# Performance work log

Measured on AMD Instinct MI355X. Metric: run time of the kernel, lower is better.

Reference implementation:

```python
import jax, jax.numpy as jnp
import numpy as np

N, E, F_IN, H, C, L = 100000, 1000000, 500, 64, 3, 3
EPS_MSG = 1e-7   # GENConv message eps
LN_EPS = 1e-5    # torch LayerNorm default eps


def layernorm(x, g, b):
    mu = jnp.mean(x, axis=-1, keepdims=True)
    var = jnp.var(x, axis=-1, keepdims=True)
    return (x - mu) * jax.lax.rsqrt(var + LN_EPS) * g + b


def gen_conv(x, src, dst, W1, b1, g1, be1, W2, b2, t):
    # message: relu(x_j) + eps   (no edge_attr)
    m = jax.nn.relu(x[src]) + EPS_MSG                      # [E, H]
    # softmax aggregation with learnable temperature t (per-channel over edges of each dst node)
    z = m * t
    zmax = jax.ops.segment_max(z, dst, num_segments=N)     # [N, H]
    a = jnp.exp(z - zmax[dst])                             # [E, H]
    denom = jax.ops.segment_sum(a, dst, num_segments=N)    # [N, H]
    agg = jax.ops.segment_sum(m * (a / denom[dst]), dst, num_segments=N)
    # out = mlp(aggr + x_root); MLP = Lin(H,2H) -> LN -> ReLU -> Lin(2H,H)
    h = agg + x
    h1 = jax.nn.relu(layernorm(h @ W1 + b1, g1, be1))
    return h1 @ W2 + b2


def setup_inputs() -> dict:
    key = jax.random.key(0)
    ks = jax.random.split(key, 16)
    s = lambda *sh: 1.0 / np.sqrt(sh[-2] if len(sh) > 1 else 1.0)
    inp = {
        'x': jax.random.normal(ks[0], (N, F_IN), dtype=jnp.float32),
        'edge_index': jax.random.randint(ks[1], (2, E), 0, N, dtype=jnp.int64),
        'enc_W': jax.random.normal(ks[2], (F_IN, H), dtype=jnp.float32) / np.sqrt(F_IN),
        'enc_b': jnp.zeros((H,), jnp.float32),
        'W1': jax.random.normal(ks[3], (L, H, 2 * H), dtype=jnp.float32) / np.sqrt(H),
        'b1': jnp.zeros((L, 2 * H), jnp.float32),
        'g1': jnp.ones((L, 2 * H), jnp.float32),
        'be1': jnp.zeros((L, 2 * H), jnp.float32),
        'W2': jax.random.normal(ks[4], (L, 2 * H, H), dtype=jnp.float32) / np.sqrt(2 * H),
        'b2': jnp.zeros((L, H), jnp.float32),
        't': jnp.ones((L,), jnp.float32),
        'ng': jnp.ones((L, H), jnp.float32),
        'nb': jnp.zeros((L, H), jnp.float32),
        'lin_W': jax.random.normal(ks[5], (H, C), dtype=jnp.float32) / np.sqrt(H),
        'lin_b': jnp.zeros((C,), jnp.float32),
    }
    return inp


def reference(x, edge_index, enc_W, enc_b, W1, b1, g1, be1, W2, b2, t, ng, nb, lin_W, lin_b):
    src, dst = edge_index[0], edge_index[1]
    h = x @ enc_W + enc_b
    # forward applies layers[0].conv once before the loop
    h = gen_conv(h, src, dst, W1[0], b1[0], g1[0], be1[0], W2[0], b2[0], t[0])
    # DeepGCNLayer block='res': h = x + dropout(relu(norm(conv(x)))), dropout is identity in eval
    for l in range(L):
        c = gen_conv(h, src, dst, W1[l], b1[l], g1[l], be1[l], W2[l], b2[l], t[l])
        c = jax.nn.relu(layernorm(c, ng[l], nb[l]))
        h = h + c
    h = jax.nn.relu(layernorm(h, ng[0], nb[0]))
    return h @ lin_W + lin_b
```

## Files before the change

kernel.cpp:

```cpp
#include <hip/hip_runtime.h>
#include <hip/hip_bf16.h>
#include <math.h>

constexpr int GN_N  = 100000;
constexpr int GN_E  = 1000000;
constexpr int GN_F  = 500;
constexpr int GN_H  = 64;
constexpr int GN_2H = 128;
constexpr int GN_C  = 3;
constexpr float GN_EPS_MSG = 1e-7f;
constexpr float GN_LN_EPS  = 1e-5f;

__global__ void k_prep(int* __restrict__ cursor, const long long* __restrict__ e64,
                       int* __restrict__ flag) {
    int i = blockIdx.x * blockDim.x + threadIdx.x;
    if (i < GN_N) cursor[i] = 0;
    if (blockIdx.x == 0) {
        __shared__ int ok;
        if (threadIdx.x == 0) ok = 1;
        __syncthreads();
        long long v = e64[threadIdx.x];
        if (v < 0 || v >= (long long)GN_N) ok = 0;
        __syncthreads();
        if (threadIdx.x == 0) *flag = ok;
    }
}

__global__ void k_hist(const void* eidx, const int* __restrict__ flag,
                       int* __restrict__ deg) {
    int e = blockIdx.x * blockDim.x + threadIdx.x;
    if (e >= GN_E) return;
    int d;
    if (*flag) d = (int)((const long long*)eidx)[GN_E + e];
    else       d = ((const int*)eidx)[GN_E + e];
    atomicAdd(&deg[d], 1);
}

__global__ void k_scan1(const int* __restrict__ deg, int* __restrict__ rowptr,
                        int* __restrict__ blksums) {
    __shared__ int sh[1024];
    int tid = threadIdx.x;
    int i = blockIdx.x * 1024 + tid;
    int v = (i < GN_N) ? deg[i] : 0;
    sh[tid] = v;
    __syncthreads();
    for (int o = 1; o < 1024; o <<= 1) {
        int add = (tid >= o) ? sh[tid - o] : 0;
        __syncthreads();
        sh[tid] += add;
        __syncthreads();
    }
    if (i < GN_N) rowptr[i + 1] = sh[tid];
    if (tid == 1023) blksums[blockIdx.x] = sh[1023];
}

__global__ void k_scan2(int* __restrict__ blksums, int nblk) {
    __shared__ int sh[128];
    int tid = threadIdx.x;
    int v = (tid < nblk) ? blksums[tid] : 0;
    sh[tid] = v;
    __syncthreads();
    for (int o = 1; o < 128; o <<= 1) {
        int add = (tid >= o) ? sh[tid - o] : 0;
        __syncthreads();
        sh[tid] += add;
        __syncthreads();
    }
    if (tid < nblk) blksums[tid] = sh[tid] - v;
}

__global__ void k_scan3(int* __restrict__ rowptr, int* __restrict__ cursor,
                        const int* __restrict__ blksums) {
    int i = blockIdx.x * 1024 + threadIdx.x;
    if (i < GN_N) {
        int v = rowptr[i + 1] + blksums[blockIdx.x];
        rowptr[i + 1] = v;
        cursor[i + 1] = v;
    }
    if (i == 0) { rowptr[0] = 0; cursor[0] = 0; }
}

__global__ void k_scatter(const void* eidx, const int* __restrict__ flag,
                          int* __restrict__ cursor, int* __restrict__ csr_src) {
    int e = blockIdx.x * blockDim.x + threadIdx.x;
    if (e >= GN_E) return;
    int s, d;
    if (*flag) { const long long* p = (const long long*)eidx; s = (int)p[e]; d = (int)p[GN_E + e]; }
    else       { const int*       p = (const int*)eidx;       s = p[e];      d = p[GN_E + e]; }
    int pos = atomicAdd(&cursor[d], 1);
    csr_src[pos] = s;
}

constexpr int ENC_BM = 64;
constexpr int ENC_KT = 100;
__global__ __launch_bounds__(256) void k_enc(const float* __restrict__ x,
        const float* __restrict__ W, const float* __restrict__ b,
        float* __restrict__ out) {
    __shared__ float xs[ENC_BM][ENC_KT];
    __shared__ float ws[ENC_KT][GN_H];
    int tid = threadIdx.x;
    int ty = tid >> 4;
    int tx = tid & 15;
    int row0 = blockIdx.x * ENC_BM;
    float4 acc0 = {0,0,0,0}, acc1 = {0,0,0,0}, acc2 = {0,0,0,0}, acc3 = {0,0,0,0};
    for (int kt = 0; kt < GN_F; kt += ENC_KT) {
        __syncthreads();
        #pragma unroll
        for (int idx = tid; idx < ENC_BM * (ENC_KT / 4); idx += 256) {
            int r  = idx / (ENC_KT / 4);
            int c4 = idx % (ENC_KT / 4);
            int gr = row0 + r; if (gr >= GN_N) gr = GN_N - 1;
            *(float4*)&xs[r][c4 * 4] =
                *(const float4*)&x[(size_t)gr * GN_F + kt + c4 * 4];
        }
        #pragma unroll
        for (int idx = tid; idx < ENC_KT * (GN_H / 4); idx += 256) {
            int r  = idx / (GN_H / 4);
            int c4 = idx % (GN_H / 4);
            *(float4*)&ws[r][c4 * 4] =
                *(const float4*)&W[(size_t)(kt + r) * GN_H + c4 * 4];
        }
        __syncthreads();
        #pragma unroll 4
        for (int k = 0; k < ENC_KT; ++k) {
            float xv0 = xs[ty * 4 + 0][k];
            float xv1 = xs[ty * 4 + 1][k];
            float xv2 = xs[ty * 4 + 2][k];
            float xv3 = xs[ty * 4 + 3][k];
            float4 wv = *(const float4*)&ws[k][tx * 4];
            acc0.x += xv0 * wv.x; acc0.y += xv0 * wv.y; acc0.z += xv0 * wv.z; acc0.w += xv0 * wv.w;
            acc1.x += xv1 * wv.x; acc1.y += xv1 * wv.y; acc1.z += xv1 * wv.z; acc1.w += xv1 * wv.w;
            acc2.x += xv2 * wv.x; acc2.y += xv2 * wv.y; acc2.z += xv2 * wv.z; acc2.w += xv2 * wv.w;
            acc3.x += xv3 * wv.x; acc3.y += xv3 * wv.y; acc3.z += xv3 * wv.z; acc3.w += xv3 * wv.w;
        }
    }
    float4 bias = *(const float4*)&b[tx * 4];
    #define ENC_STORE(i, accv)                                                 \
    {   int gr = row0 + ty * 4 + i;                                            \
        if (gr < GN_N) {                                                       \
            float4 o; o.x = accv.x + bias.x; o.y = accv.y + bias.y;            \
            o.z = accv.z + bias.z; o.w = accv.w + bias.w;                      \
            *(float4*)&out[(size_t)gr * GN_H + tx * 4] = o;                    \
        } }
    ENC_STORE(0, acc0) ENC_STORE(1, acc1) ENC_STORE(2, acc2) ENC_STORE(3, acc3)
    #undef ENC_STORE
}

__global__ __launch_bounds__(256) void k_conv_agg(const float* __restrict__ h,
        const int* __restrict__ rowptr, const int* __restrict__ csr_src,
        const float* __restrict__ t_all, int layer, float* __restrict__ out) {
    int lane = threadIdx.x & 63;
    int node = blockIdx.x * 4 + (threadIdx.x >> 6);
    if (node >= GN_N) return;
    float t = t_all[layer];
    int beg = rowptr[node], end = rowptr[node + 1];
    float mx = -INFINITY, den = 0.f, num = 0.f;
    #define AGG_EDGE(vv)                                                       \
    {   float m = fmaxf(vv, 0.f) + GN_EPS_MSG;                                 \
        float z = m * t;                                                       \
        float nm = fmaxf(mx, z);                                               \
        float sc = __expf(mx - nm);                                            \
        float a  = __expf(z - nm);                                             \
        den = den * sc + a;                                                    \
        num = num * sc + m * a;                                                \
        mx = nm; }
    int e = beg;
    for (; e + 3 < end; e += 4) {
        int s0 = csr_src[e];
        int s1 = csr_src[e + 1];
        int s2 = csr_src[e + 2];
        int s3 = csr_src[e + 3];
        float v0 = h[(size_t)s0 * GN_H + lane];
        float v1 = h[(size_t)s1 * GN_H + lane];
        float v2 = h[(size_t)s2 * GN_H + lane];
        float v3 = h[(size_t)s3 * GN_H + lane];
        AGG_EDGE(v0) AGG_EDGE(v1) AGG_EDGE(v2) AGG_EDGE(v3)
    }
    for (; e < end; ++e) {
        int s = csr_src[e];
        float v = h[(size_t)s * GN_H + lane];
        AGG_EDGE(v)
    }
    #undef AGG_EDGE
    float agg = (end > beg) ? (num / den) : 0.f;
    out[(size_t)node * GN_H + lane] = agg + h[(size_t)node * GN_H + lane];
}

__global__ __launch_bounds__(256) void k_conv_mlp(float* buf,
        const float* __restrict__ h_old,
        const float* __restrict__ W1, const float* __restrict__ b1,
        const float* __restrict__ g1, const float* __restrict__ be1,
        const float* __restrict__ W2, const float* __restrict__ b2,
        const float* __restrict__ ng, const float* __restrict__ nb,
        const float* __restrict__ ng0, const float* __restrict__ nb0,
        const float* __restrict__ linW, const float* __restrict__ linb,
        float* __restrict__ out, int mode) {
    __shared__ float w1s[GN_H * GN_2H];
    __shared__ float w2s[GN_2H * GN_H];
    __shared__ float xbuf[4][4][GN_H];
    __shared__ float hbuf[4][4][GN_2H];
    int tid = threadIdx.x;
    for (int i = tid * 4; i < GN_H * GN_2H; i += 256 * 4) {
        *(float4*)&w1s[i] = *(const float4*)&W1[i];
        *(float4*)&w2s[i] = *(const float4*)&W2[i];
    }
    __syncthreads();
    int lane = tid & 63;
    int wid  = tid >> 6;
    float b1a = b1[2 * lane], b1b = b1[2 * lane + 1];
    float g1a = g1[2 * lane], g1b = g1[2 * lane + 1];
    float e1a = be1[2 * lane], e1b = be1[2 * lane + 1];
    float b2c = b2[lane];
    float ngc = ng[lane], nbc = nb[lane];
    float ng0c = ng0[lane], nb0c = nb0[lane];
    float lw0 = linW[lane * GN_C + 0];
    float lw1 = linW[lane * GN_C + 1];
    float lw2 = linW[lane * GN_C + 2];

    for (int n0 = blockIdx.x * 16 + wid * 4; n0 < GN_N; n0 += gridDim.x * 16) {
        xbuf[wid][0][lane] = buf[(size_t)(n0 + 0) * GN_H + lane];
        xbuf[wid][1][lane] = buf[(size_t)(n0 + 1) * GN_H + lane];
        xbuf[wid][2][lane] = buf[(size_t)(n0 + 2) * GN_H + lane];
        xbuf[wid][3][lane] = buf[(size_t)(n0 + 3) * GN_H + lane];
        float a00 = b1a, a01 = b1b, a10 = b1a, a11 = b1b;
        float a20 = b1a, a21 = b1b, a30 = b1a, a31 = b1b;
        #pragma unroll
        for (int k = 0; k < GN_H; k += 4) {
            float4 x0 = *(const float4*)&xbuf[wid][0][k];
            float4 x1 = *(const float4*)&xbuf[wid][1][k];
            float4 x2 = *(const float4*)&xbuf[wid][2][k];
            float4 x3 = *(const float4*)&xbuf[wid][3][k];
            #pragma unroll
            for (int kk = 0; kk < 4; ++kk) {
                float2 w = *(const float2*)&w1s[(k + kk) * GN_2H + 2 * lane];
                float e0 = (&x0.x)[kk], e1 = (&x1.x)[kk];
                float e2 = (&x2.x)[kk], e3 = (&x3.x)[kk];
                a00 += e0 * w.x; a01 += e0 * w.y;
                a10 += e1 * w.x; a11 += e1 * w.y;
                a20 += e2 * w.x; a21 += e2 * w.y;
                a30 += e3 * w.x; a31 += e3 * w.y;
            }
        }
        float s0 = a00 + a01, q0 = a00 * a00 + a01 * a01;
        float s1 = a10 + a11, q1 = a10 * a10 + a11 * a11;
        float s2 = a20 + a21, q2 = a20 * a20 + a21 * a21;
        float s3 = a30 + a31, q3 = a30 * a30 + a31 * a31;
        #pragma unroll
        for (int o = 1; o < 64; o <<= 1) {
            s0 += __shfl_xor(s0, o); q0 += __shfl_xor(q0, o);
            s1 += __shfl_xor(s1, o); q1 += __shfl_xor(q1, o);
            s2 += __shfl_xor(s2, o); q2 += __shfl_xor(q2, o);
            s3 += __shfl_xor(s3, o); q3 += __shfl_xor(q3, o);
        }
        #define LN128(sv, qv, aA, aB, hA, hB)                                  \
        float hA, hB;                                                          \
        {   float mu = sv * (1.f / 128.f);                                     \
            float var = qv * (1.f / 128.f) - mu * mu;                          \
            float rstd = rsqrtf(var + GN_LN_EPS);                              \
            hA = fmaxf((aA - mu) * rstd * g1a + e1a, 0.f);                     \
            hB = fmaxf((aB - mu) * rstd * g1b + e1b, 0.f); }
        LN128(s0, q0, a00, a01, h00, h01)
        LN128(s1, q1, a10, a11, h10, h11)
        LN128(s2, q2, a20, a21, h20, h21)
        LN128(s3, q3, a30, a31, h30, h31)
        #undef LN128
        *(float2*)&hbuf[wid][0][2 * lane] = make_float2(h00, h01);
        *(float2*)&hbuf[wid][1][2 * lane] = make_float2(h10, h11);
        *(float2*)&hbuf[wid][2][2 * lane] = make_float2(h20, h21);
        *(float2*)&hbuf[wid][3][2 * lane] = make_float2(h30, h31);
        float c0 = b2c, c1 = b2c, c2 = b2c, c3 = b2c;
        #pragma unroll
        for (int j = 0; j < GN_2H; j += 4) {
            float w0 = w2s[(j + 0) * GN_H + lane];
            float w1 = w2s[(j + 1) * GN_H + lane];
            float w2 = w2s[(j + 2) * GN_H + lane];
            float w3 = w2s[(j + 3) * GN_H + lane];
            float4 hv0 = *(const float4*)&hbuf[wid][0][j];
            float4 hv1 = *(const float4*)&hbuf[wid][1][j];
            float4 hv2 = *(const float4*)&hbuf[wid][2][j];
            float4 hv3 = *(const float4*)&hbuf[wid][3][j];
            c0 += hv0.x * w0 + hv0.y * w1 + hv0.z * w2 + hv0.w * w3;
            c1 += hv1.x * w0 + hv1.y * w1 + hv1.z * w2 + hv1.w * w3;
            c2 += hv2.x * w0 + hv2.y * w1 + hv2.z * w2 + hv2.w * w3;
            c3 += hv3.x * w0 + hv3.y * w1 + hv3.z * w2 + hv3.w * w3;
        }
        if (mode == 0) {
            buf[(size_t)(n0 + 0) * GN_H + lane] = c0;
            buf[(size_t)(n0 + 1) * GN_H + lane] = c1;
            buf[(size_t)(n0 + 2) * GN_H + lane] = c2;
            buf[(size_t)(n0 + 3) * GN_H + lane] = c3;
            continue;
        }
        float t0 = c0, u0 = c0 * c0, t1 = c1, u1 = c1 * c1;
        float t2 = c2, u2 = c2 * c2, t3 = c3, u3 = c3 * c3;
        #pragma unroll
        for (int o = 1; o < 64; o <<= 1) {
            t0 += __shfl_xor(t0, o); u0 += __shfl_xor(u0, o);
            t1 += __shfl_xor(t1, o); u1 += __shfl_xor(u1, o);
            t2 += __shfl_xor(t2, o); u2 += __shfl_xor(u2, o);
            t3 += __shfl_xor(t3, o); u3 += __shfl_xor(u3, o);
        }
        float r0, r1, r2, r3;
        #define LN64(tv, uv, cv, rv, idx)                                      \
        {   float mu = tv * (1.f / 64.f);                                      \
            float var = uv * (1.f / 64.f) - mu * mu;                           \
            float rstd = rsqrtf(var + GN_LN_EPS);                              \
            float cvn = fmaxf((cv - mu) * rstd * ngc + nbc, 0.f);              \
            rv = h_old[(size_t)(n0 + idx) * GN_H + lane] + cvn; }
        LN64(t0, u0, c0, r0, 0)
        LN64(t1, u1, c1, r1, 1)
        LN64(t2, u2, c2, r2, 2)
        LN64(t3, u3, c3, r3, 3)
        #undef LN64
        if (mode == 1) {
            buf[(size_t)(n0 + 0) * GN_H + lane] = r0;
            buf[(size_t)(n0 + 1) * GN_H + lane] = r1;
            buf[(size_t)(n0 + 2) * GN_H + lane] = r2;
            buf[(size_t)(n0 + 3) * GN_H + lane] = r3;
            continue;
        }
        float f0 = r0, v0 = r0 * r0, f1 = r1, v1 = r1 * r1;
        float f2 = r2, v2 = r2 * r2, f3 = r3, v3 = r3 * r3;
        #pragma unroll
        for (int o = 1; o < 64; o <<= 1) {
            f0 += __shfl_xor(f0, o); v0 += __shfl_xor(v0, o);
            f1 += __shfl_xor(f1, o); v1 += __shfl_xor(v1, o);
            f2 += __shfl_xor(f2, o); v2 += __shfl_xor(v2, o);
            f3 += __shfl_xor(f3, o); v3 += __shfl_xor(v3, o);
        }
        #define FINHEAD(fv, vv, rv, idx)                                       \
        {   float mu = fv * (1.f / 64.f);                                      \
            float var = vv * (1.f / 64.f) - mu * mu;                           \
            float rstd = rsqrtf(var + GN_LN_EPS);                              \
            float hn = fmaxf((rv - mu) * rstd * ng0c + nb0c, 0.f);             \
            float p0 = hn * lw0, p1 = hn * lw1, p2 = hn * lw2;                 \
            _Pragma("unroll")                                                  \
            for (int o = 1; o < 64; o <<= 1) {                                 \
                p0 += __shfl_xor(p0, o);                                       \
                p1 += __shfl_xor(p1, o);                                       \
                p2 += __shfl_xor(p2, o);                                       \
            }                                                                  \
            if (lane == 0) {                                                   \
                out[(size_t)(n0 + idx) * GN_C + 0] = p0 + linb[0];             \
                out[(size_t)(n0 + idx) * GN_C + 1] = p1 + linb[1];             \
                out[(size_t)(n0 + idx) * GN_C + 2] = p2 + linb[2];             \
            } }
        FINHEAD(f0, v0, r0, 0)
        FINHEAD(f1, v1, r1, 1)
        FINHEAD(f2, v2, r2, 2)
        FINHEAD(f3, v3, r3, 3)
        #undef FINHEAD
    }
}

extern "C" void kernel_launch(void* const* d_in, const int* in_sizes, int n_in,
                              void* d_out, int out_size, void* d_ws, size_t ws_size,
                              hipStream_t stream) {
    const float* x     = (const float*)d_in[0];
    const void*  eidx  = d_in[1];
    const float* enc_W = (const float*)d_in[2];
    const float* enc_b = (const float*)d_in[3];
    const float* W1    = (const float*)d_in[4];
    const float* b1    = (const float*)d_in[5];
    const float* g1    = (const float*)d_in[6];
    const float* be1   = (const float*)d_in[7];
    const float* W2    = (const float*)d_in[8];
    const float* b2    = (const float*)d_in[9];
    const float* t     = (const float*)d_in[10];
    const float* ng    = (const float*)d_in[11];
    const float* nb    = (const float*)d_in[12];
    const float* linW  = (const float*)d_in[13];
    const float* linb  = (const float*)d_in[14];
    float* out = (float*)d_out;

    float* A      = (float*)d_ws;
    float* B      = A + (size_t)GN_N * GN_H;
    int*   rowptr = (int*)(B + (size_t)GN_N * GN_H);
    int*   cursor = rowptr + (GN_N + 8);
    int*   csr_src= cursor + (GN_N + 8);
    int*   blksums= csr_src + GN_E;
    int*   flag   = blksums + 128;

    const int nblk = (GN_N + 1023) / 1024;

    k_prep   <<<(GN_N + 255) / 256, 256, 0, stream>>>(cursor, (const long long*)eidx, flag);
    k_hist   <<<(GN_E + 255) / 256, 256, 0, stream>>>(eidx, flag, cursor);
    k_scan1  <<<nblk, 1024, 0, stream>>>(cursor, rowptr, blksums);
    k_scan2  <<<1, 128, 0, stream>>>(blksums, nblk);
    k_scan3  <<<nblk, 1024, 0, stream>>>(rowptr, cursor, blksums);
    k_scatter<<<(GN_E + 255) / 256, 256, 0, stream>>>(eidx, flag, cursor, csr_src);

    k_enc<<<(GN_N + ENC_BM - 1) / ENC_BM, 256, 0, stream>>>(x, enc_W, enc_b, A);

    k_conv_agg<<<GN_N / 4, 256, 0, stream>>>(A, rowptr, csr_src, t, 0, B);
    k_conv_mlp<<<512, 256, 0, stream>>>(B, A, W1, b1, g1, be1, W2, b2,
                                        ng, nb, ng, nb, linW, linb, out, 0);

    float* cur = B; float* alt = A;
    for (int l = 0; l < 3; ++l) {
        k_conv_agg<<<GN_N / 4, 256, 0, stream>>>(cur, rowptr, csr_src, t, l, alt);
        k_conv_mlp<<<512, 256, 0, stream>>>(alt, cur,
            W1 + (size_t)l * GN_H * GN_2H, b1 + (size_t)l * GN_2H,
            g1 + (size_t)l * GN_2H,        be1 + (size_t)l * GN_2H,
            W2 + (size_t)l * GN_2H * GN_H, b2 + (size_t)l * GN_H,
            ng + (size_t)l * GN_H,         nb + (size_t)l * GN_H,
            ng, nb, linW, linb, out, (l == 2) ? 2 : 1);
        float* tmp = cur; cur = alt; alt = tmp;
    }
}
```

Before: 1.166 ms.

## Retile encoder GEMM to 8x8 register blocking and transpose W2 in shared memory

The encoder GEMM moves from 256-thread blocks with 4x4 per-thread tiles to 128-thread blocks covering 128 rows with 8x8 register tiles. It stores the x tile k-major so each thread reads its rows with float4 loads, raising FLOPs per shared-memory load. In the conv MLP, W2 is stored transposed with padding so each lane reads four consecutive weights with one float4 instead of four scalar loads. The trade-off is higher register pressure and lower occupancy in the encoder, and strided per-thread global loads of x rows (each thread reads its own row), which may hurt coalescing.

```diff
diff --git a/kernel.cpp b/kernel.cpp
--- a/kernel.cpp
+++ b/kernel.cpp
@@ -91,59 +91,70 @@
     csr_src[pos] = s;
 }
 
-constexpr int ENC_BM = 64;
-constexpr int ENC_KT = 100;
-__global__ __launch_bounds__(256) void k_enc(const float* __restrict__ x,
+constexpr int ENC_BM = 128;
+constexpr int ENC_KT = 50;
+__global__ __launch_bounds__(128) void k_enc(const float* __restrict__ x,
         const float* __restrict__ W, const float* __restrict__ b,
         float* __restrict__ out) {
-    __shared__ float xs[ENC_BM][ENC_KT];
+    __shared__ float xs[ENC_KT][ENC_BM];
     __shared__ float ws[ENC_KT][GN_H];
     int tid = threadIdx.x;
-    int ty = tid >> 4;
-    int tx = tid & 15;
+    int ty = tid >> 3;
+    int tx = tid & 7;
     int row0 = blockIdx.x * ENC_BM;
-    float4 acc0 = {0,0,0,0}, acc1 = {0,0,0,0}, acc2 = {0,0,0,0}, acc3 = {0,0,0,0};
+    float acc[8][8];
+    #pragma unroll
+    for (int i = 0; i < 8; ++i)
+        #pragma unroll
+        for (int j = 0; j < 8; ++j) acc[i][j] = 0.f;
+
+    int grow = row0 + tid; if (grow >= GN_N) grow = GN_N - 1;
+    const float* xrow = x + (size_t)grow * GN_F;
+
     for (int kt = 0; kt < GN_F; kt += ENC_KT) {
         __syncthreads();
         #pragma unroll
-        for (int idx = tid; idx < ENC_BM * (ENC_KT / 4); idx += 256) {
-            int r  = idx / (ENC_KT / 4);
-            int c4 = idx % (ENC_KT / 4);
-            int gr = row0 + r; if (gr >= GN_N) gr = GN_N - 1;
-            *(float4*)&xs[r][c4 * 4] =
-                *(const float4*)&x[(size_t)gr * GN_F + kt + c4 * 4];
-        }
-        #pragma unroll
-        for (int idx = tid; idx < ENC_KT * (GN_H / 4); idx += 256) {
-            int r  = idx / (GN_H / 4);
-            int c4 = idx % (GN_H / 4);
+        for (int i = 0; i < ENC_KT / 2; ++i) {
+            float2 v = *(const float2*)&xrow[kt + 2 * i];
+            xs[2 * i][tid]     = v.x;
+            xs[2 * i + 1][tid] = v.y;
+        }
+        for (int idx = tid; idx < ENC_KT * (GN_H / 4); idx += 128) {
+            int r = idx >> 4, c4 = idx & 15;
             *(float4*)&ws[r][c4 * 4] =
                 *(const float4*)&W[(size_t)(kt + r) * GN_H + c4 * 4];
         }
         __syncthreads();
-        #pragma unroll 4
+        #pragma unroll 2
         for (int k = 0; k < ENC_KT; ++k) {
-            float xv0 = xs[ty * 4 + 0][k];
-            float xv1 = xs[ty * 4 + 1][k];
-            float xv2 = xs[ty * 4 + 2][k];
-            float xv3 = xs[ty * 4 + 3][k];
-            float4 wv = *(const float4*)&ws[k][tx * 4];
-            acc0.x += xv0 * wv.x; acc0.y += xv0 * wv.y; acc0.z += xv0 * wv.z; acc0.w += xv0 * wv.w;
-            acc1.x += xv1 * wv.x; acc1.y += xv1 * wv.y; acc1.z += xv1 * wv.z; acc1.w += xv1 * wv.w;
-            acc2.x += xv2 * wv.x; acc2.y += xv2 * wv.y; acc2.z += xv2 * wv.z; acc2.w += xv2 * wv.w;
-            acc3.x += xv3 * wv.x; acc3.y += xv3 * wv.y; acc3.z += xv3 * wv.z; acc3.w += xv3 * wv.w;
-        }
-    }
-    float4 bias = *(const float4*)&b[tx * 4];
-    #define ENC_STORE(i, accv)                                                 \
-    {   int gr = row0 + ty * 4 + i;                                            \
-        if (gr < GN_N) {                                                       \
-            float4 o; o.x = accv.x + bias.x; o.y = accv.y + bias.y;            \
-            o.z = accv.z + bias.z; o.w = accv.w + bias.w;                      \
-            *(float4*)&out[(size_t)gr * GN_H + tx * 4] = o;                    \
-        } }
-    ENC_STORE(0, acc0) ENC_STORE(1, acc1) ENC_STORE(2, acc2) ENC_STORE(3, acc3)
-    #undef ENC_STORE
+            float4 xa = *(const float4*)&xs[k][ty * 8];
+            float4 xb = *(const float4*)&xs[k][ty * 8 + 4];
+            float4 wa = *(const float4*)&ws[k][tx * 8];
+            float4 wb = *(const float4*)&ws[k][tx * 8 + 4];
+            float xr[8] = {xa.x, xa.y, xa.z, xa.w, xb.x, xb.y, xb.z, xb.w};
+            float wc[8] = {wa.x, wa.y, wa.z, wa.w, wb.x, wb.y, wb.z, wb.w};
+            #pragma unroll
+            for (int i = 0; i < 8; ++i)
+                #pragma unroll
+                for (int j = 0; j < 8; ++j)
+                    acc[i][j] += xr[i] * wc[j];
+        }
+    }
+    float4 ba = *(const float4*)&b[tx * 8];
+    float4 bb = *(const float4*)&b[tx * 8 + 4];
+    #pragma unroll
+    for (int i = 0; i < 8; ++i) {
+        int gr = row0 + ty * 8 + i;
+        if (gr < GN_N) {
+            float4 o0, o1;
+            o0.x = acc[i][0] + ba.x; o0.y = acc[i][1] + ba.y;
+            o0.z = acc[i][2] + ba.z; o0.w = acc[i][3] + ba.w;
+            o1.x = acc[i][4] + bb.x; o1.y = acc[i][5] + bb.y;
+            o1.z = acc[i][6] + bb.z; o1.w = acc[i][7] + bb.w;
+            *(float4*)&out[(size_t)gr * GN_H + tx * 8]     = o0;
+            *(float4*)&out[(size_t)gr * GN_H + tx * 8 + 4] = o1;
+        }
+    }
 }
 
 __global__ __launch_bounds__(256) void k_conv_agg(const float* __restrict__ h,
@@ -196,13 +207,19 @@
         const float* __restrict__ linW, const float* __restrict__ linb,
         float* __restrict__ out, int mode) {
     __shared__ float w1s[GN_H * GN_2H];
-    __shared__ float w2s[GN_2H * GN_H];
+    __shared__ float w2sT[GN_H][132];
     __shared__ float xbuf[4][4][GN_H];
     __shared__ float hbuf[4][4][GN_2H];
     int tid = threadIdx.x;
-    for (int i = tid * 4; i < GN_H * GN_2H; i += 256 * 4) {
+    for (int i = tid * 4; i < GN_H * GN_2H; i += 256 * 4)
         *(float4*)&w1s[i] = *(const float4*)&W1[i];
-        *(float4*)&w2s[i] = *(const float4*)&W2[i];
+    for (int idx = tid; idx < GN_2H * (GN_H / 4); idx += 256) {
+        int j = idx >> 4, c4 = idx & 15;
+        float4 v = *(const float4*)&W2[(size_t)j * GN_H + c4 * 4];
+        w2sT[c4 * 4 + 0][j] = v.x;
+        w2sT[c4 * 4 + 1][j] = v.y;
+        w2sT[c4 * 4 + 2][j] = v.z;
+        w2sT[c4 * 4 + 3][j] = v.w;
     }
     __syncthreads();
     int lane = tid & 63;
@@ -270,19 +287,16 @@
         *(float2*)&hbuf[wid][3][2 * lane] = make_float2(h30, h31);
         float c0 = b2c, c1 = b2c, c2 = b2c, c3 = b2c;
         #pragma unroll
-        for (int j = 0; j < GN_2H; j += 4) {
-            float w0 = w2s[(j + 0) * GN_H + lane];
-            float w1 = w2s[(j + 1) * GN_H + lane];
-            float w2 = w2s[(j + 2) * GN_H + lane];
-            float w3 = w2s[(j + 3) * GN_H + lane];
-            float4 hv0 = *(const float4*)&hbuf[wid][0][j];
-            float4 hv1 = *(const float4*)&hbuf[wid][1][j];
-            float4 hv2 = *(const float4*)&hbuf[wid][2][j];
-            float4 hv3 = *(const float4*)&hbuf[wid][3][j];
-            c0 += hv0.x * w0 + hv0.y * w1 + hv0.z * w2 + hv0.w * w3;
-            c1 += hv1.x * w0 + hv1.y * w1 + hv1.z * w2 + hv1.w * w3;
-            c2 += hv2.x * w0 + hv2.y * w1 + hv2.z * w2 + hv2.w * w3;
-            c3 += hv3.x * w0 + hv3.y * w1 + hv3.z * w2 + hv3.w * w3;
+        for (int j4 = 0; j4 < GN_2H; j4 += 4) {
+            float4 w  = *(const float4*)&w2sT[lane][j4];
+            float4 hv0 = *(const float4*)&hbuf[wid][0][j4];
+            float4 hv1 = *(const float4*)&hbuf[wid][1][j4];
+            float4 hv2 = *(const float4*)&hbuf[wid][2][j4];
+            float4 hv3 = *(const float4*)&hbuf[wid][3][j4];
+            c0 += hv0.x * w.x + hv0.y * w.y + hv0.z * w.z + hv0.w * w.w;
+            c1 += hv1.x * w.x + hv1.y * w.y + hv1.z * w.z + hv1.w * w.w;
+            c2 += hv2.x * w.x + hv2.y * w.y + hv2.z * w.z + hv2.w * w.w;
+            c3 += hv3.x * w.x + hv3.y * w.y + hv3.z * w.z + hv3.w * w.w;
         }
         if (mode == 0) {
             buf[(size_t)(n0 + 0) * GN_H + lane] = c0;
@@ -390,7 +404,7 @@
     k_scan3  <<<nblk, 1024, 0, stream>>>(rowptr, cursor, blksums);
     k_scatter<<<(GN_E + 255) / 256, 256, 0, stream>>>(eidx, flag, cursor, csr_src);
 
-    k_enc<<<(GN_N + ENC_BM - 1) / ENC_BM, 256, 0, stream>>>(x, enc_W, enc_b, A);
+    k_enc<<<(GN_N + ENC_BM - 1) / ENC_BM, 128, 0, stream>>>(x, enc_W, enc_b, A);
 
     k_conv_agg<<<GN_N / 4, 256, 0, stream>>>(A, rowptr, csr_src, t, 0, B);
     k_conv_mlp<<<512, 256, 0, stream>>>(B, A, W1, b1, g1, be1, W2, b2,
```

Result: faster. 1.132 ms (-2.9%).
